# Kernel tuning notes

Hardware: AMD Instinct MI355X
Metric: run time of the kernel (lower is better)

## Reference

```python
import jax, jax.numpy as jnp
import numpy as np
import math

H = 16          # head_count
D = 1024        # model_dim
DT = 100        # topic_dim
DH = D // H     # dim_per_head


def _lin(x, W, b):
    return x @ W.T + b


def _shape(x, B):
    # [B, L, D] -> [B, H, L, DH]
    return x.reshape(B, -1, H, DH).transpose(0, 2, 1, 3)


def setup_inputs() -> dict:
    key = jax.random.key(0)
    ks = jax.random.split(key, 20)
    B, L = 4, 1024
    s = 0.02
    inp = {
        'key': jax.random.normal(ks[0], (B, L, D), jnp.float32),
        'value': jax.random.normal(ks[1], (B, L, D), jnp.float32),
        'query': jax.random.normal(ks[2], (B, L, D), jnp.float32),
        'mask': jax.random.randint(ks[3], (B, L, L), 0, 2).astype(bool),
        'topic_vec': jax.random.normal(ks[4], (B, L, DT), jnp.float32),
        'Wq': jax.random.normal(ks[5], (D, D), jnp.float32) * s,
        'bq': jnp.zeros((D,), jnp.float32),
        'Wk': jax.random.normal(ks[6], (D, D), jnp.float32) * s,
        'bk': jnp.zeros((D,), jnp.float32),
        'Wv': jax.random.normal(ks[7], (D, D), jnp.float32) * s,
        'bv': jnp.zeros((D,), jnp.float32),
        'Wtk': jax.random.normal(ks[8], (D, D), jnp.float32) * s,
        'btk': jnp.zeros((D,), jnp.float32),
        'Wtv': jax.random.normal(ks[9], (D, DT), jnp.float32) * s,
        'btv': jnp.zeros((D,), jnp.float32),
        'Wtw': jax.random.normal(ks[10], (H, 3 * D), jnp.float32) * s,
        'btw': jnp.zeros((H,), jnp.float32),
        'Wo': jax.random.normal(ks[11], (D, D), jnp.float32) * s,
        'bo': jnp.zeros((D,), jnp.float32),
    }
    return inp


def reference(key, value, query, mask, topic_vec,
              Wq, bq, Wk, bk, Wv, bv, Wtk, btk, Wtv, btv, Wtw, btw, Wo, bo):
    B = key.shape[0]
    # content and topic projections
    q_lin = _lin(query, Wq, bq)          # [B, L, D]
    k_lin = _lin(key, Wk, bk)
    v_lin = _lin(value, Wv, bv)
    tk_lin = _lin(key, Wtk, btk)         # topic keys from key states
    tv_lin = _lin(topic_vec, Wtv, btv)   # topic queries from topic distribution

    q = _shape(q_lin, B) / math.sqrt(DH)   # [B, H, Lq, DH]
    k = _shape(k_lin, B)
    v = _shape(v_lin, B)
    tk = _shape(tk_lin, B)
    tq = _shape(tv_lin, B) / math.sqrt(DH)

    scores = jnp.einsum('bhqd,bhkd->bhqk', q, k)          # content scores
    topic_scores = jnp.einsum('bhqd,bhkd->bhqk', tq, tk)  # topic scores

    # per-query, per-head mixing gate from concatenated projections (3*D -> H)
    gate = jax.nn.sigmoid(_lin(jnp.concatenate([q_lin, tk_lin, tv_lin], axis=-1), Wtw, btw))  # [B, L, H]
    p = gate.transpose(0, 2, 1)[..., None]                # [B, H, Lq, 1]
    scores = (1.0 - p) * scores + p * topic_scores

    # masked_fill(mask, -1e18), mask broadcast over heads
    scores = jnp.where(mask[:, None, :, :], -1e18, scores)
    attn = jax.nn.softmax(scores, axis=-1)
    # dropout is identity at eval time
    ctx = jnp.einsum('bhqk,bhkd->bhqd', attn, v)
    ctx = ctx.transpose(0, 2, 1, 3).reshape(B, -1, D)     # unshape
    return ctx @ Wo.T + bo
```

## Files before the change

kernel.cpp:

```cpp
#include <hip/hip_runtime.h>
#include <hip/hip_bf16.h>

#define BB 4
#define LL 1024
#define DD 1024
#define HH 16
#define DHH 64
#define DTT 100
#define ML (BB*LL)
#define LOG2E 1.4426950408889634f

typedef float f32x4 __attribute__((ext_vector_type(4)));
typedef short s16x8 __attribute__((ext_vector_type(8)));

__device__ __forceinline__ unsigned short f2bf(float x) {
    unsigned u = __builtin_bit_cast(unsigned, x);
    return (unsigned short)((u + 0x7FFFu + ((u >> 16) & 1u)) >> 16);
}
__device__ __forceinline__ unsigned short f2bf_fast(float x) {
    return (unsigned short)((__builtin_bit_cast(unsigned, x) + 0x8000u) >> 16);
}
__device__ __forceinline__ unsigned cvt_pk_bf16(float lo, float hi) {
    unsigned r;
    asm("v_cvt_pk_bf16_f32 %0, %1, %2" : "=v"(r) : "v"(lo), "v"(hi));
    return r;
}
__device__ __forceinline__ float bflo(unsigned u) { return __builtin_bit_cast(float, u << 16); }
__device__ __forceinline__ float bfhi(unsigned u) { return __builtin_bit_cast(float, u & 0xFFFF0000u); }
__device__ __forceinline__ int4 pack_bf16x8(float4 x0, float4 x1) {
    int4 o;
    o.x = cvt_pk_bf16(x0.x, x0.y); o.y = cvt_pk_bf16(x0.z, x0.w);
    o.z = cvt_pk_bf16(x1.x, x1.y); o.w = cvt_pk_bf16(x1.z, x1.w);
    return o;
}

__global__ __launch_bounds__(256)
void conv_fused(const float* __restrict__ w0, const float* __restrict__ w1,
                const float* __restrict__ w2, const float* __restrict__ w3,
                const float* __restrict__ w4, unsigned short* __restrict__ wd,
                const float* __restrict__ wtw, unsigned short* __restrict__ wtwd,
                const float* __restrict__ wtv, unsigned short* __restrict__ wtvd,
                const float* __restrict__ topic, unsigned short* __restrict__ topicd,
                const int* __restrict__ mask, unsigned long long* __restrict__ MB) {
    const int bx = blockIdx.x, tid = threadIdx.x;
    if (bx < 2560) {
        const int which = bx >> 9;
        const float* src;
        switch (which) {
            case 0:  src = w0; break;
            case 1:  src = w1; break;
            case 2:  src = w2; break;
            case 3:  src = w3; break;
            default: src = w4; break;
        }
        unsigned short* dst = wd + (size_t)which * DD * DD;
        const int idx = (bx & 511) * 256 + tid;
        float4 f0 = *(const float4*)(src + (size_t)idx * 8);
        float4 f1 = *(const float4*)(src + (size_t)idx * 8 + 4);
        *(int4*)(dst + (size_t)idx * 8) = pack_bf16x8(f0, f1);
    } else if (bx < 2584) {
        const int idx = (bx - 2560) * 256 + tid;
        float4 f0 = *(const float4*)(wtw + (size_t)idx * 8);
        float4 f1 = *(const float4*)(wtw + (size_t)idx * 8 + 4);
        *(int4*)(wtwd + (size_t)idx * 8) = pack_bf16x8(f0, f1);
    } else if (bx < 2648) {
        const int idx = (bx - 2584) * 256 + tid;
        const int r = idx >> 4, c0 = (idx & 15) * 8;
        unsigned short o[8];
        #pragma unroll
        for (int j = 0; j < 8; j++) {
            int c = c0 + j;
            o[j] = (c < DTT) ? f2bf(wtv[(size_t)r * DTT + c]) : (unsigned short)0;
        }
        int4 v;
        v.x = o[0] | ((unsigned)o[1] << 16);
        v.y = o[2] | ((unsigned)o[3] << 16);
        v.z = o[4] | ((unsigned)o[5] << 16);
        v.w = o[6] | ((unsigned)o[7] << 16);
        *(int4*)(wtvd + (size_t)r * 128 + c0) = v;
    } else if (bx < 2904) {
        const int idx = (bx - 2648) * 256 + tid;
        const int r = idx >> 4, c0 = (idx & 15) * 8;
        unsigned short o[8];
        #pragma unroll
        for (int j = 0; j < 8; j++) {
            int c = c0 + j;
            o[j] = (c < DTT) ? f2bf(topic[(size_t)r * DTT + c]) : (unsigned short)0;
        }
        int4 v;
        v.x = o[0] | ((unsigned)o[1] << 16);
        v.y = o[2] | ((unsigned)o[3] << 16);
        v.z = o[4] | ((unsigned)o[5] << 16);
        v.w = o[6] | ((unsigned)o[7] << 16);
        *(int4*)(topicd + (size_t)r * 128 + c0) = v;
    } else {
        const int ww = (bx - 2904) * 4 + (tid >> 6);
        const int lane = tid & 63;
        int v = mask[(size_t)ww * 64 + lane];
        unsigned long long bits = __ballot(v != 0);
        if (lane == 0) MB[ww] = bits;
    }
}

struct GArg { const void* A; const unsigned short* W; const float* bias; void* C; int mode; };

#define LOADW(s0_,s1_,s2_,s3_,kk) \
    s0_ = *(const int4*)(Wb + (kk)); \
    s1_ = *(const int4*)(Wb + (kk) + wstep); \
    s2_ = *(const int4*)(Wb + (kk) + 2 * wstep); \
    s3_ = *(const int4*)(Wb + (kk) + 3 * wstep);
#define STOREW(s0_,s1_,s2_,s3_) \
    *(int4*)(bsl)         = s0_; \
    *(int4*)(bsl + 4096)  = s1_; \
    *(int4*)(bsl + 8192)  = s2_; \
    *(int4*)(bsl + 12288) = s3_;
#define LOADA16(s0_,s1_,s2_,s3_,kk) \
    s0_ = *(const int4*)(Ab16 + (kk)); \
    s1_ = *(const int4*)(Ab16 + (kk) + wstep); \
    s2_ = *(const int4*)(Ab16 + (kk) + 2 * wstep); \
    s3_ = *(const int4*)(Ab16 + (kk) + 3 * wstep);
#define STOREA16(s0_,s1_,s2_,s3_) \
    *(int4*)(asl)         = s0_; \
    *(int4*)(asl + 4096)  = s1_; \
    *(int4*)(asl + 8192)  = s2_; \
    *(int4*)(asl + 12288) = s3_;
#define LOADA32(q0_,q1_,q2_,q3_,q4_,q5_,q6_,q7_,kk) \
    q0_ = *(const float4*)(Af32 + (kk));             q1_ = *(const float4*)(Af32 + (kk) + 4); \
    q2_ = *(const float4*)(Af32 + (kk) + wstep);     q3_ = *(const float4*)(Af32 + (kk) + wstep + 4); \
    q4_ = *(const float4*)(Af32 + (kk) + 2 * wstep); q5_ = *(const float4*)(Af32 + (kk) + 2 * wstep + 4); \
    q6_ = *(const float4*)(Af32 + (kk) + 3 * wstep); q7_ = *(const float4*)(Af32 + (kk) + 3 * wstep + 4);
#define STOREA32(q0_,q1_,q2_,q3_,q4_,q5_,q6_,q7_) \
    *(int4*)(asl)         = pack_bf16x8(q0_, q1_); \
    *(int4*)(asl + 4096)  = pack_bf16x8(q2_, q3_); \
    *(int4*)(asl + 8192)  = pack_bf16x8(q4_, q5_); \
    *(int4*)(asl + 12288) = pack_bf16x8(q6_, q7_);
#define GEMM_COMPUTE(ABASE, BBASE) \
    _Pragma("unroll") \
    for (int ks = 0; ks < 2; ks++) { \
        s16x8 af[4], bf[4]; \
        _Pragma("unroll") \
        for (int m = 0; m < 4; m++) { \
            const int ra = wr * 64 + m * 16 + c; \
            af[m] = *(const s16x8*)((ABASE) + ra * 128 + (((ks * 4 + g) ^ (ra & 7)) << 4)); \
            const int rb = wc * 64 + m * 16 + c; \
            bf[m] = *(const s16x8*)((BBASE) + rb * 128 + (((ks * 4 + g) ^ (rb & 7)) << 4)); \
        } \
        _Pragma("unroll") \
        for (int m = 0; m < 4; m++) \
            _Pragma("unroll") \
            for (int n = 0; n < 4; n++) \
                acc[m][n] = __builtin_amdgcn_mfma_f32_16x16x32_bf16(af[m], bf[n], acc[m][n], 0, 0, 0); \
    }

template<int AFP32>
__global__ __launch_bounds__(256, 3)
void gemm_mfma(GArg a0, GArg a1, GArg a2, GArg a3, int N, int K) {
    __shared__ char lds[32768];
    char* As = lds;
    char* Bs = lds + 16384;

    const int nb = gridDim.x * gridDim.y * gridDim.z;
    const int flat = blockIdx.x + gridDim.x * (blockIdx.y + gridDim.y * blockIdx.z);
    const int wid = (flat & 7) * (nb >> 3) + (flat >> 3);
    const int bx = wid % gridDim.x;
    const int rem = wid / gridDim.x;
    const int by = rem % gridDim.y;
    const int bz = rem / gridDim.y;

    GArg a;
    switch (bz) {
        case 0:  a = a0; break;
        case 1:  a = a1; break;
        case 2:  a = a2; break;
        default: a = a3; break;
    }

    const int tid = threadIdx.x, w = tid >> 6, l = tid & 63;
    const int g = l >> 4, c = l & 15;
    const int wr = w >> 1, wc = w & 1;
    const int bm = by * 128, bn = bx * 128;

    const int r0 = tid >> 3, sl = tid & 7;
    char* const asl = As + r0 * 128 + ((sl ^ (r0 & 7)) << 4);
    char* const bsl = Bs + r0 * 128 + ((sl ^ (r0 & 7)) << 4);
    const size_t wstep = (size_t)32 * K;
    const unsigned short* const Wb   = a.W + (size_t)(bn + r0) * K + sl * 8;
    const unsigned short* const Ab16 = (const unsigned short*)a.A + (size_t)(bm + r0) * K + sl * 8;
    const float* const           Af32 = (const float*)a.A + (size_t)(bm + r0) * K + sl * 8;

    f32x4 acc[4][4];
    #pragma unroll
    for (int m = 0; m < 4; m++)
        #pragma unroll
        for (int n = 0; n < 4; n++)
            #pragma unroll
            for (int j = 0; j < 4; j++) acc[m][n][j] = 0.f;

    int4 pw0, pw1, pw2, pw3;
    int4 pa0, pa1, pa2, pa3;
    float4 qa0, qa1, qa2, qa3, qa4, qa5, qa6, qa7;
    LOADW(pw0, pw1, pw2, pw3, 0)
    if (AFP32) { LOADA32(qa0, qa1, qa2, qa3, qa4, qa5, qa6, qa7, 0) }
    else       { LOADA16(pa0, pa1, pa2, pa3, 0) }

    for (int k0 = 0; k0 < K; k0 += 64) {
        __syncthreads();
        if (AFP32) { STOREA32(qa0, qa1, qa2, qa3, qa4, qa5, qa6, qa7) }
        else       { STOREA16(pa0, pa1, pa2, pa3) }
        STOREW(pw0, pw1, pw2, pw3)
        {
            const int kn = (k0 + 64 < K) ? (k0 + 64) : 0;
            LOADW(pw0, pw1, pw2, pw3, kn)
            if (AFP32) { LOADA32(qa0, qa1, qa2, qa3, qa4, qa5, qa6, qa7, kn) }
            else       { LOADA16(pa0, pa1, pa2, pa3, kn) }
        }
        __syncthreads();
        GEMM_COMPUTE(As, Bs)
    }

    const int mode = a.mode;
    if (mode == 0) {
        float* C = (float*)a.C;
        #pragma unroll
        for (int n = 0; n < 4; n++) {
            const int col = bn + wc * 64 + n * 16 + c;
            const float bv = a.bias[col];
            #pragma unroll
            for (int m = 0; m < 4; m++) {
                const int row = bm + wr * 64 + m * 16 + g * 4;
                #pragma unroll
                for (int j = 0; j < 4; j++)
                    C[(size_t)(row + j) * N + col] = acc[m][n][j] + bv;
            }
        }
    } else if (mode == 1) {
        unsigned short* C = (unsigned short*)a.C;
        #pragma unroll
        for (int n = 0; n < 4; n++) {
            const int col = bn + wc * 64 + n * 16 + c;
            const float bv = a.bias[col];
            #pragma unroll
            for (int m = 0; m < 4; m++) {
                const int row = bm + wr * 64 + m * 16 + g * 4;
                #pragma unroll
                for (int j = 0; j < 4; j++)
                    C[(size_t)(row + j) * N + col] = f2bf(acc[m][n][j] + bv);
            }
        }
    } else if (mode == 2 || mode == 3) {
        unsigned short* C = (unsigned short*)a.C;
        const int off = (mode == 2) ? 0 : 64;
        #pragma unroll
        for (int n = 0; n < 4; n++) {
            const int col = bn + wc * 64 + n * 16 + c;
            const float bv = a.bias[col];
            const int h = col >> 6, d = col & 63;
            #pragma unroll
            for (int m = 0; m < 4; m++) {
                const int row = bm + wr * 64 + m * 16 + g * 4;
                #pragma unroll
                for (int j = 0; j < 4; j++) {
                    const int rr = row + j;
                    C[((size_t)((rr >> 10) * HH + h) * LL + (rr & 1023)) * 128 + off + d] =
                        f2bf(acc[m][n][j] + bv);
                }
            }
        }
    } else {
        unsigned short* C = (unsigned short*)a.C;
        #pragma unroll
        for (int n = 0; n < 4; n++) {
            const int col = bn + wc * 64 + n * 16 + c;
            const float bv = a.bias[col];
            const int h = col >> 6, d = col & 63;
            #pragma unroll
            for (int m = 0; m < 4; m++) {
                const int row = bm + wr * 64 + m * 16 + g * 4;
                unsigned lo = cvt_pk_bf16(acc[m][n][0] + bv, acc[m][n][1] + bv);
                unsigned hi = cvt_pk_bf16(acc[m][n][2] + bv, acc[m][n][3] + bv);
                unsigned long long pk = (unsigned long long)lo | ((unsigned long long)hi << 32);
                *(unsigned long long*)(C + ((size_t)((row >> 10) * HH + h) * 64 + d) * LL + (row & 1023)) = pk;
            }
        }
    }
}

__global__ __launch_bounds__(256)
void gate_kernel(const unsigned short* __restrict__ QLb,
                 const unsigned short* __restrict__ KCb,
                 const unsigned short* __restrict__ TVLb,
                 const unsigned short* __restrict__ Wtwb,
                 const float* __restrict__ btw, float* __restrict__ GATE) {
    const int t = threadIdx.x;
    const int q = t >> 6, sub = t & 63, row = sub >> 4, h = sub & 15;
    const int row_g = blockIdx.x * 4 + row;
    const int b = row_g >> 10, l = row_g & 1023;

    float acc = 0.f;
    const unsigned short* wp = Wtwb + h * 3 * DD + q * 768;
    #pragma unroll 4
    for (int cc = 0; cc < 96; cc++) {
        const int i = q * 768 + cc * 8;
        const unsigned short* xp;
        if (i < 1024) {
            xp = QLb + (size_t)row_g * DD + i;
        } else if (i < 2048) {
            const int j = i - 1024;
            xp = KCb + ((size_t)(b * HH + (j >> 6)) * LL + l) * 128 + 64 + (j & 63);
        } else {
            xp = TVLb + (size_t)row_g * DD + (i - 2048);
        }
        int4 xv = *(const int4*)xp;
        int4 wv = *(const int4*)(wp + cc * 8);
        const unsigned xs[4] = {(unsigned)xv.x, (unsigned)xv.y, (unsigned)xv.z, (unsigned)xv.w};
        const unsigned ws[4] = {(unsigned)wv.x, (unsigned)wv.y, (unsigned)wv.z, (unsigned)wv.w};
        #pragma unroll
        for (int jj = 0; jj < 4; jj++) {
            acc = fmaf(bflo(xs[jj]), bflo(ws[jj]), acc);
            acc = fmaf(bfhi(xs[jj]), bfhi(ws[jj]), acc);
        }
    }
    __shared__ float part[4][4][16];
    part[q][row][h] = acc;
    __syncthreads();
    if (t < 64) {
        float s = part[0][row][h] + part[1][row][h] + part[2][row][h] + part[3][row][h] + btw[h];
        GATE[(size_t)row_g * HH + h] = 1.f / (1.f + __expf(-s));
    }
}

__global__ __launch_bounds__(256, 3)
void attn_mfma(const unsigned short* __restrict__ QLb,
               const unsigned short* __restrict__ TVLb,
               const float* __restrict__ GATE,
               const unsigned short* __restrict__ KC,
               const unsigned short* __restrict__ VT,
               const unsigned long long* __restrict__ MB,
               unsigned short* __restrict__ CTb) {
    __shared__ char lds[32768];
    char* kc_l = lds;
    char* vt_l = lds + 16384;
    char* p_l  = lds + 24576;

    const int tid = threadIdx.x, w = tid >> 6, l = tid & 63;
    const int g = l >> 4, c = l & 15;
    const int flat = blockIdx.y * gridDim.x + blockIdx.x;
    const int wid = (flat & 7) * 128 + (flat >> 3);
    const int qb = wid & 15, bh = wid >> 4;
    const int b = bh >> 4, h = bh & 15;
    const int q0 = qb * 64;

    const size_t kcg = (size_t)bh * LL * 128;
    const size_t vtg = (size_t)bh * 64 * LL;

    const int kr = tid >> 4, ks = tid & 15;
    const size_t kgo = (size_t)kr * 128 + ks * 8;
    char* const klb = kc_l + kr * 256 + ((ks ^ (kr & 7)) << 4);
    const int vr = tid >> 3, vs = tid & 7;
    const size_t vgo = (size_t)vr * LL + vs * 8;
    char* const vlb = vt_l + vr * 128 + ((vs ^ (vr & 7)) << 4);

    int4 pk0, pk1, pk2, pk3, pv0, pv1;
    {
        const unsigned short* kp = KC + kcg + kgo;
        pk0 = *(const int4*)kp;
        pk1 = *(const int4*)(kp + 16 * 128);
        pk2 = *(const int4*)(kp + 32 * 128);
        pk3 = *(const int4*)(kp + 48 * 128);
        const unsigned short* vp = VT + vtg + vgo;
        pv0 = *(const int4*)vp;
        pv1 = *(const int4*)(vp + 32 * LL);
    }

    {
        const size_t rowbase = (size_t)b * LL + q0 + kr;
        const unsigned short* qsrc =
            (ks < 8 ? QLb : TVLb) + rowbase * DD + h * DHH + (ks & 7) * 8;
        const float* gp = GATE + rowbase * HH + h;
        #pragma unroll
        for (int i = 0; i < 4; i++) {
            const float p = gp[(size_t)i * 16 * HH];
            const float sc = (ks < 8 ? 1.f - p : p) * (0.125f * LOG2E);
            int4 v = *(const int4*)(qsrc + (size_t)i * 16 * DD);
            int4 o;
            o.x = cvt_pk_bf16(bflo((unsigned)v.x) * sc, bfhi((unsigned)v.x) * sc);
            o.y = cvt_pk_bf16(bflo((unsigned)v.y) * sc, bfhi((unsigned)v.y) * sc);
            o.z = cvt_pk_bf16(bflo((unsigned)v.z) * sc, bfhi((unsigned)v.z) * sc);
            o.w = cvt_pk_bf16(bflo((unsigned)v.w) * sc, bfhi((unsigned)v.w) * sc);
            *(int4*)(klb + i * 4096) = o;
        }
    }
    __syncthreads();
    s16x8 qf[4];
    const int ql = w * 16 + c;
    #pragma unroll
    for (int kss = 0; kss < 4; kss++) {
        int t = kss * 4 + g;
        qf[kss] = *(s16x8*)(kc_l + ql * 256 + ((t ^ (ql & 7)) << 4));
    }

    f32x4 ctx[4], la;
    #pragma unroll
    for (int ct = 0; ct < 4; ct++)
        #pragma unroll
        for (int j = 0; j < 4; j++) ctx[ct][j] = 0.f;
    #pragma unroll
    for (int j = 0; j < 4; j++) la[j] = 0.f;
    float m_r[4] = {-1e18f, -1e18f, -1e18f, -1e18f};

    s16x8 ones;
    #pragma unroll
    for (int j = 0; j < 8; j++) ones[j] = (short)0x3F80;

    const unsigned long long* mbq = MB + ((size_t)b * LL + q0 + w * 16 + g * 4) * 16;

    for (int kt = 0; kt < 16; kt++) {
        __syncthreads();
        *(int4*)(klb)          = pk0;
        *(int4*)(klb + 4096)   = pk1;
        *(int4*)(klb + 8192)   = pk2;
        *(int4*)(klb + 12288)  = pk3;
        *(int4*)(vlb)          = pv0;
        *(int4*)(vlb + 4096)   = pv1;
        {
            const unsigned short* kp = KC + kcg + (size_t)(kt + 1) * (64 * 128) + kgo;
            pk0 = *(const int4*)kp;
            pk1 = *(const int4*)(kp + 16 * 128);
            pk2 = *(const int4*)(kp + 32 * 128);
            pk3 = *(const int4*)(kp + 48 * 128);
            const unsigned short* vp = VT + vtg + (size_t)(kt + 1) * 64 + vgo;
            pv0 = *(const int4*)vp;
            pv1 = *(const int4*)(vp + 32 * LL);
        }
        __syncthreads();

        f32x4 sf[4];
        #pragma unroll
        for (int ct = 0; ct < 4; ct++) {
            f32x4 acc;
            #pragma unroll
            for (int j = 0; j < 4; j++) acc[j] = 0.f;
            const int rk = ct * 16 + c;
            #pragma unroll
            for (int kss = 0; kss < 4; kss++) {
                int t = kss * 4 + g;
                s16x8 kf = *(s16x8*)(kc_l + rk * 256 + ((t ^ (rk & 7)) << 4));
                acc = __builtin_amdgcn_mfma_f32_16x16x32_bf16(qf[kss], kf, acc, 0, 0, 0);
            }
            sf[ct] = acc;
        }

        #pragma unroll
        for (int r = 0; r < 4; r++) {
            const unsigned long long mw = mbq[r * 16 + kt];
            const unsigned mlo = (unsigned)mw >> c;
            const unsigned mhi = (unsigned)(mw >> 32) >> c;
            float s0 = (mlo & 1u)         ? -1e18f : sf[0][r];
            float s1 = ((mlo >> 16) & 1u) ? -1e18f : sf[1][r];
            float s2 = (mhi & 1u)         ? -1e18f : sf[2][r];
            float s3 = ((mhi >> 16) & 1u) ? -1e18f : sf[3][r];
            float mx = fmaxf(fmaxf(s0, s1), fmaxf(s2, s3));
            #pragma unroll
            for (int off = 1; off < 16; off <<= 1) mx = fmaxf(mx, __shfl_xor(mx, off, 16));
            float mn = fmaxf(m_r[r], mx);
            float cf = exp2f(m_r[r] - mn);
            m_r[r] = mn;
            #pragma unroll
            for (int ct = 0; ct < 4; ct++) ctx[ct][r] *= cf;
            la[r] *= cf;
            const int qrow = g * 4 + r;
            char* pb = p_l + w * 2048 + qrow * 128;
            const int sub = (c & 7) * 2, hi = c >> 3, sw = qrow & 7;
            *(unsigned short*)(pb + (((0 + hi) ^ sw) << 4) + sub) = f2bf_fast(exp2f(s0 - mn));
            *(unsigned short*)(pb + (((2 + hi) ^ sw) << 4) + sub) = f2bf_fast(exp2f(s1 - mn));
            *(unsigned short*)(pb + (((4 + hi) ^ sw) << 4) + sub) = f2bf_fast(exp2f(s2 - mn));
            *(unsigned short*)(pb + (((6 + hi) ^ sw) << 4) + sub) = f2bf_fast(exp2f(s3 - mn));
        }

        char* pb = p_l + w * 2048;
        s16x8 pa0 = *(s16x8*)(pb + c * 128 + (((0 + g) ^ (c & 7)) << 4));
        s16x8 pa1 = *(s16x8*)(pb + c * 128 + (((4 + g) ^ (c & 7)) << 4));
        #pragma unroll
        for (int ct = 0; ct < 4; ct++) {
            const int dv = ct * 16 + c;
            s16x8 v0 = *(s16x8*)(vt_l + dv * 128 + (((0 + g) ^ (dv & 7)) << 4));
            s16x8 v1 = *(s16x8*)(vt_l + dv * 128 + (((4 + g) ^ (dv & 7)) << 4));
            ctx[ct] = __builtin_amdgcn_mfma_f32_16x16x32_bf16(pa0, v0, ctx[ct], 0, 0, 0);
            ctx[ct] = __builtin_amdgcn_mfma_f32_16x16x32_bf16(pa1, v1, ctx[ct], 0, 0, 0);
        }
        la = __builtin_amdgcn_mfma_f32_16x16x32_bf16(pa0, ones, la, 0, 0, 0);
        la = __builtin_amdgcn_mfma_f32_16x16x32_bf16(pa1, ones, la, 0, 0, 0);
    }

    #pragma unroll
    for (int r = 0; r < 4; r++) {
        const float inv = 1.f / la[r];
        const int q = q0 + w * 16 + g * 4 + r;
        unsigned short* dst = CTb + ((size_t)b * LL + q) * DD + h * DHH + c;
        dst[0]  = f2bf(ctx[0][r] * inv);
        dst[16] = f2bf(ctx[1][r] * inv);
        dst[32] = f2bf(ctx[2][r] * inv);
        dst[48] = f2bf(ctx[3][r] * inv);
    }
}

extern "C" void kernel_launch(void* const* d_in, const int* in_sizes, int n_in,
                              void* d_out, int out_size, void* d_ws, size_t ws_size,
                              hipStream_t stream) {
    const float* key   = (const float*)d_in[0];
    const float* value = (const float*)d_in[1];
    const float* query = (const float*)d_in[2];
    const int*   mask  = (const int*)d_in[3];
    const float* topic = (const float*)d_in[4];
    const float* Wq  = (const float*)d_in[5];  const float* bq  = (const float*)d_in[6];
    const float* Wk  = (const float*)d_in[7];  const float* bk  = (const float*)d_in[8];
    const float* Wv  = (const float*)d_in[9];  const float* bv  = (const float*)d_in[10];
    const float* Wtk = (const float*)d_in[11]; const float* btk = (const float*)d_in[12];
    const float* Wtv = (const float*)d_in[13]; const float* btv = (const float*)d_in[14];
    const float* Wtw = (const float*)d_in[15]; const float* btw = (const float*)d_in[16];
    const float* Wo  = (const float*)d_in[17]; const float* bo  = (const float*)d_in[18];
    float* out = (float*)d_out;

    const size_t NTOK = (size_t)ML * DD;
    unsigned short* Wqb   = (unsigned short*)d_ws;
    unsigned short* Wkb   = Wqb  + (size_t)DD * DD;
    unsigned short* Wvb   = Wkb  + (size_t)DD * DD;
    unsigned short* Wtkb  = Wvb  + (size_t)DD * DD;
    unsigned short* Wob   = Wtkb + (size_t)DD * DD;
    unsigned short* Wtvb  = Wob  + (size_t)DD * DD;
    unsigned short* Wtwb  = Wtvb + (size_t)DD * 128;
    unsigned short* topicb= Wtwb + (size_t)HH * 3 * DD;
    unsigned short* QLb   = topicb + (size_t)ML * 128;
    unsigned short* TVLb  = QLb  + NTOK;
    unsigned short* CTb   = TVLb + NTOK;
    unsigned short* KCb   = CTb  + NTOK;
    unsigned short* VTb   = KCb  + (size_t)BB * HH * LL * 128;
    float* GATE           = (float*)(VTb + (size_t)BB * HH * 64 * LL);
    unsigned long long* MBp = (unsigned long long*)(GATE + (size_t)ML * HH);

    conv_fused<<<19288, 256, 0, stream>>>(Wq, Wk, Wv, Wtk, Wo, Wqb,
                                          Wtw, Wtwb, Wtv, Wtvb, topic, topicb,
                                          mask, MBp);

    gemm_mfma<1><<<dim3(DD / 128, ML / 128, 4), 256, 0, stream>>>(
        GArg{query, Wqb,  bq,  QLb, 1},
        GArg{key,   Wkb,  bk,  KCb, 2},
        GArg{value, Wvb,  bv,  VTb, 4},
        GArg{key,   Wtkb, btk, KCb, 3},
        DD, DD);
    gemm_mfma<0><<<dim3(DD / 128, ML / 128, 1), 256, 0, stream>>>(
        GArg{topicb, Wtvb, btv, TVLb, 1},
        GArg{topicb, Wtvb, btv, TVLb, 1},
        GArg{topicb, Wtvb, btv, TVLb, 1},
        GArg{topicb, Wtvb, btv, TVLb, 1},
        DD, 128);

    gate_kernel<<<ML / 4, 256, 0, stream>>>(QLb, KCb, TVLb, Wtwb, btw, GATE);

    attn_mfma<<<dim3(LL / 64, BB * HH), 256, 0, stream>>>(QLb, TVLb, GATE, KCb, VTb, MBp, CTb);

    gemm_mfma<0><<<dim3(DD / 128, ML / 128, 1), 256, 0, stream>>>(
        GArg{CTb, Wob, bo, out, 0},
        GArg{CTb, Wob, bo, out, 0},
        GArg{CTb, Wob, bo, out, 0},
        GArg{CTb, Wob, bo, out, 0},
        DD, DD);
}
```

Measured before the change: 212.4 us.

## Compute transposed score tiles so each lane owns one query row in softmax

```diff
diff --git a/kernel.cpp b/kernel.cpp
--- a/kernel.cpp
+++ b/kernel.cpp
@@ -406,13 +406,13 @@
         for (int j = 0; j < 4; j++) ctx[ct][j] = 0.f;
     #pragma unroll
     for (int j = 0; j < 4; j++) la[j] = 0.f;
-    float m_r[4] = {-1e18f, -1e18f, -1e18f, -1e18f};
+    float m_s = -1e18f;
 
     s16x8 ones;
     #pragma unroll
     for (int j = 0; j < 8; j++) ones[j] = (short)0x3F80;
 
-    const unsigned long long* mbq = MB + ((size_t)b * LL + q0 + w * 16 + g * 4) * 16;
+    const unsigned long long* mbq = MB + ((size_t)b * LL + q0 + w * 16 + c) * 16;
 
     for (int kt = 0; kt < 16; kt++) {
         __syncthreads();
@@ -445,36 +445,54 @@
             for (int kss = 0; kss < 4; kss++) {
                 int t = kss * 4 + g;
                 s16x8 kf = *(s16x8*)(kc_l + rk * 256 + ((t ^ (rk & 7)) << 4));
-                acc = __builtin_amdgcn_mfma_f32_16x16x32_bf16(qf[kss], kf, acc, 0, 0, 0);
+                acc = __builtin_amdgcn_mfma_f32_16x16x32_bf16(kf, qf[kss], acc, 0, 0, 0);
             }
             sf[ct] = acc;
         }
 
-        #pragma unroll
-        for (int r = 0; r < 4; r++) {
-            const unsigned long long mw = mbq[r * 16 + kt];
-            const unsigned mlo = (unsigned)mw >> c;
-            const unsigned mhi = (unsigned)(mw >> 32) >> c;
-            float s0 = (mlo & 1u)         ? -1e18f : sf[0][r];
-            float s1 = ((mlo >> 16) & 1u) ? -1e18f : sf[1][r];
-            float s2 = (mhi & 1u)         ? -1e18f : sf[2][r];
-            float s3 = ((mhi >> 16) & 1u) ? -1e18f : sf[3][r];
-            float mx = fmaxf(fmaxf(s0, s1), fmaxf(s2, s3));
-            #pragma unroll
-            for (int off = 1; off < 16; off <<= 1) mx = fmaxf(mx, __shfl_xor(mx, off, 16));
-            float mn = fmaxf(m_r[r], mx);
-            float cf = exp2f(m_r[r] - mn);
-            m_r[r] = mn;
-            #pragma unroll
-            for (int ct = 0; ct < 4; ct++) ctx[ct][r] *= cf;
-            la[r] *= cf;
-            const int qrow = g * 4 + r;
-            char* pb = p_l + w * 2048 + qrow * 128;
-            const int sub = (c & 7) * 2, hi = c >> 3, sw = qrow & 7;
-            *(unsigned short*)(pb + (((0 + hi) ^ sw) << 4) + sub) = f2bf_fast(exp2f(s0 - mn));
-            *(unsigned short*)(pb + (((2 + hi) ^ sw) << 4) + sub) = f2bf_fast(exp2f(s1 - mn));
-            *(unsigned short*)(pb + (((4 + hi) ^ sw) << 4) + sub) = f2bf_fast(exp2f(s2 - mn));
-            *(unsigned short*)(pb + (((6 + hi) ^ sw) << 4) + sub) = f2bf_fast(exp2f(s3 - mn));
+        {
+            const unsigned long long mw = mbq[kt];
+            const unsigned ms0 = (unsigned)(mw >> (g * 4));
+            const unsigned ms1 = (unsigned)(mw >> (g * 4 + 32));
+            #pragma unroll
+            for (int ct = 0; ct < 4; ct++) {
+                const unsigned mm = (ct & 2) ? ms1 : ms0;
+                const int sh = (ct & 1) ? 16 : 0;
+                #pragma unroll
+                for (int j = 0; j < 4; j++)
+                    if ((mm >> (sh + j)) & 1u) sf[ct][j] = -1e18f;
+            }
+            float t0 = fmaxf(fmaxf(sf[0][0], sf[0][1]), fmaxf(sf[0][2], sf[0][3]));
+            float t1 = fmaxf(fmaxf(sf[1][0], sf[1][1]), fmaxf(sf[1][2], sf[1][3]));
+            float t2 = fmaxf(fmaxf(sf[2][0], sf[2][1]), fmaxf(sf[2][2], sf[2][3]));
+            float t3 = fmaxf(fmaxf(sf[3][0], sf[3][1]), fmaxf(sf[3][2], sf[3][3]));
+            float mx = fmaxf(fmaxf(t0, t1), fmaxf(t2, t3));
+            mx = fmaxf(mx, __shfl_xor(mx, 16));
+            mx = fmaxf(mx, __shfl_xor(mx, 32));
+            const float mn = fmaxf(m_s, mx);
+            const float cf = exp2f(m_s - mn);
+            m_s = mn;
+
+            const float cr0 = __shfl(cf, g * 4 + 0, 16);
+            const float cr1 = __shfl(cf, g * 4 + 1, 16);
+            const float cr2 = __shfl(cf, g * 4 + 2, 16);
+            const float cr3 = __shfl(cf, g * 4 + 3, 16);
+            #pragma unroll
+            for (int ct = 0; ct < 4; ct++) {
+                ctx[ct][0] *= cr0; ctx[ct][1] *= cr1;
+                ctx[ct][2] *= cr2; ctx[ct][3] *= cr3;
+            }
+            la[0] *= cr0; la[1] *= cr1; la[2] *= cr2; la[3] *= cr3;
+
+            char* pw = p_l + w * 2048 + c * 128;
+            #pragma unroll
+            for (int ct = 0; ct < 4; ct++) {
+                const unsigned lo = cvt_pk_bf16(exp2f(sf[ct][0] - mn), exp2f(sf[ct][1] - mn));
+                const unsigned hi = cvt_pk_bf16(exp2f(sf[ct][2] - mn), exp2f(sf[ct][3] - mn));
+                const unsigned long long pkv =
+                    (unsigned long long)lo | ((unsigned long long)hi << 32);
+                *(unsigned long long*)(pw + (((ct * 2 + (g >> 1)) ^ (c & 7)) << 4) + ((g & 1) << 3)) = pkv;
+            }
         }
 
         char* pb = p_l + w * 2048;
```

After: 196.2 us. -7.6%, faster.
